# Kernel optimization log

Measured on AMD Instinct MI355X. Metric: run time of the kernel, lower is better.

The kernel has to match this reference:

```python
import jax, jax.numpy as jnp
import numpy as np

B, N, D = 32, 4096, 256
H, DH, S = 8, 64, 16
DI = H * DH          # dim_inner = 512
HID = 1024           # max(dim, hidden_dim)
ITERS = 3
EPS = 1e-8
SCALE = D ** (-0.5)  # NOTE: original uses dim, not dim_head


def _ln(x, g, b):
    m = jnp.mean(x, axis=-1, keepdims=True)
    v = jnp.mean((x - m) ** 2, axis=-1, keepdims=True)
    return (x - m) * jax.lax.rsqrt(v + 1e-5) * g + b


def _lin(x, W, b):  # torch layout: W [out, in]
    return x @ W.T + b


def setup_inputs() -> dict:
    key = jax.random.key(0)
    ks = jax.random.split(key, 32)

    def p(i, shape, s=0.02):
        return jax.random.normal(ks[i], shape, dtype=jnp.float32) * s

    return {
        "x": jax.random.normal(ks[0], (B, N, D), dtype=jnp.float32),
        "slots_noise": jax.random.normal(ks[1], (B, S, D), dtype=jnp.float32),
        "slots_mu": p(2, (1, 1, D), 1.0),
        "slots_logsigma": p(3, (1, 1, D)),
        "ln_in_g": jnp.ones((D,), jnp.float32), "ln_in_b": jnp.zeros((D,), jnp.float32),
        "ln_s_g": jnp.ones((D,), jnp.float32), "ln_s_b": jnp.zeros((D,), jnp.float32),
        "ln_ff_g": jnp.ones((D,), jnp.float32), "ln_ff_b": jnp.zeros((D,), jnp.float32),
        "Wq": p(4, (DI, D)), "bq": jnp.zeros((DI,), jnp.float32),
        "Wk": p(5, (DI, D)), "bk": jnp.zeros((DI,), jnp.float32),
        "Wv": p(6, (DI, D)), "bv": jnp.zeros((DI,), jnp.float32),
        "Wc": p(7, (D, DI)), "bc": jnp.zeros((D,), jnp.float32),
        "gru_wih": p(8, (3 * D, D)), "gru_whh": p(9, (3 * D, D)),
        "gru_bih": jnp.zeros((3 * D,), jnp.float32), "gru_bhh": jnp.zeros((3 * D,), jnp.float32),
        "W1": p(10, (HID, D)), "b1": jnp.zeros((HID,), jnp.float32),
        "W2": p(11, (D, HID)), "b2": jnp.zeros((D,), jnp.float32),
    }


def reference(x, slots_noise, slots_mu, slots_logsigma,
              ln_in_g, ln_in_b, ln_s_g, ln_s_b, ln_ff_g, ln_ff_b,
              Wq, bq, Wk, bk, Wv, bv, Wc, bc,
              gru_wih, gru_whh, gru_bih, gru_bhh,
              W1, b1, W2, b2):
    slots = slots_mu + jnp.exp(slots_logsigma) * slots_noise  # [B,S,D]
    xn = _ln(x, ln_in_g, ln_in_b)
    k = _lin(xn, Wk, bk).reshape(B, N, H, DH)  # [B,N,H,DH]
    v = _lin(xn, Wv, bv).reshape(B, N, H, DH)

    for _ in range(ITERS):
        slots_prev = slots
        sn = _ln(slots, ln_s_g, ln_s_b)
        q = _lin(sn, Wq, bq).reshape(B, S, H, DH)             # [B,S,H,DH]
        logits = jnp.einsum('bihd,bjhd->bhij', q, k) * SCALE  # [B,H,S,N]
        attn = jax.nn.softmax(logits, axis=-1) + EPS
        attn = attn / jnp.sum(attn, axis=-1, keepdims=True)
        upd = jnp.einsum('bhij,bjhd->bihd', attn, v).reshape(B, S, DI)
        upd = _lin(upd, Wc, bc)                               # [B,S,D]
        # GRUCell (torch gate order r, z, n)
        gi = _lin(upd.reshape(-1, D), gru_wih, gru_bih)
        gh = _lin(slots_prev.reshape(-1, D), gru_whh, gru_bhh)
        ir, iz, inn = jnp.split(gi, 3, axis=-1)
        hr, hz, hn = jnp.split(gh, 3, axis=-1)
        r = jax.nn.sigmoid(ir + hr)
        z = jax.nn.sigmoid(iz + hz)
        n = jnp.tanh(inn + r * hn)
        slots = ((1.0 - z) * n + z * slots_prev.reshape(-1, D)).reshape(B, S, D)
        slots = slots + _lin(jax.nn.relu(_lin(_ln(slots, ln_ff_g, ln_ff_b), W1, b1)), W2, b2)
    return slots
```

## Files before the change

kernel.cpp:

```cpp
#include <hip/hip_runtime.h>
#include <stdint.h>

#define B_   32
#define N_   4096
#define D_   256
#define H_   8
#define S_   16
#define DI_  512
#define HID_ 1024
#define CH_  8
#define NCHUNK_ 512
#define SCALE_ 0.0625f

typedef short  short8 __attribute__((ext_vector_type(8)));
typedef float  f32x4  __attribute__((ext_vector_type(4)));

__device__ __forceinline__ unsigned short f2bf(float x){
  union { float f; unsigned u; } v; v.f = x;
  unsigned r = v.u + 0x7FFFu + ((v.u >> 16) & 1u);
  return (unsigned short)(r >> 16);
}

__device__ __forceinline__ void gld16(const void* g, void* l){
  __builtin_amdgcn_global_load_lds(
      (const __attribute__((address_space(1))) unsigned int*)g,
      (__attribute__((address_space(3))) unsigned int*)l, 16, 0, 0);
}

#define FMA4(acc, a, Wm) do { (acc)[0] += (a)*(Wm).x; (acc)[1] += (a)*(Wm).y; (acc)[2] += (a)*(Wm).z; (acc)[3] += (a)*(Wm).w; } while(0)

__global__ void k_badws(float* out){ out[blockIdx.x*256 + threadIdx.x] = 1e9f; }

__global__ __launch_bounds__(256) void k_init_slots(
    const float* __restrict__ noise, const float* __restrict__ mu,
    const float* __restrict__ lsig, float* __restrict__ slots)
{
  int i = blockIdx.x*256 + threadIdx.x;
  int d = i & 255;
  slots[i] = mu[d] + expf(lsig[d]) * noise[i];
}

__global__ __launch_bounds__(256) void k_transpose(
    const float* __restrict__ src, float* __restrict__ dst, int R, int C)
{
  __shared__ float t[32][33];
  int c0 = blockIdx.x*32, r0 = blockIdx.y*32;
  int tx = threadIdx.x, ty = threadIdx.y;
  for (int j = 0; j < 32; j += 8){
    int r = r0 + ty + j, c = c0 + tx;
    if (r < R && c < C) t[ty+j][tx] = src[(size_t)r*C + c];
  }
  __syncthreads();
  for (int j = 0; j < 32; j += 8){
    int c = c0 + ty + j, r = r0 + tx;
    if (c < C && r < R) dst[(size_t)c*R + r] = t[tx][ty+j];
  }
}

__global__ __launch_bounds__(256) void k_ln_x(
    const float* __restrict__ x, const float* __restrict__ g, const float* __restrict__ bb,
    unsigned short* __restrict__ xn, unsigned short* __restrict__ xnT)
{
  __shared__ __align__(16) char tile[32768];
  const int blk = blockIdx.x;
  const int b  = blk >> 6;
  const int n0 = (blk & 63) * 64;
  const int t = threadIdx.x;
  const int lane = t & 63;
  const int w = t >> 6;
  float4 gv = *(const float4*)&g[lane*4];
  float4 bv = *(const float4*)&bb[lane*4];
#pragma unroll 1
  for (int it = 0; it < 16; ++it){
    const int nl = w*16 + it;
    const size_t row = (size_t)b*N_ + n0 + nl;
    float4 xv = *(const float4*)&x[row*256 + lane*4];
    float s = xv.x + xv.y + xv.z + xv.w;
    float q = xv.x*xv.x + xv.y*xv.y + xv.z*xv.z + xv.w*xv.w;
#pragma unroll
    for (int m = 1; m < 64; m <<= 1){ s += __shfl_xor(s, m); q += __shfl_xor(q, m); }
    float mean = s * 0.00390625f;
    float var  = q * 0.00390625f - mean*mean;
    float rs = rsqrtf(var + 1e-5f);
    unsigned short u0 = f2bf((xv.x-mean)*rs*gv.x + bv.x);
    unsigned short u1 = f2bf((xv.y-mean)*rs*gv.y + bv.y);
    unsigned short u2 = f2bf((xv.z-mean)*rs*gv.z + bv.z);
    unsigned short u3 = f2bf((xv.w-mean)*rs*gv.w + bv.w);
    uint2 pk; pk.x = (unsigned)u0 | ((unsigned)u1 << 16); pk.y = (unsigned)u2 | ((unsigned)u3 << 16);
    *(uint2*)&xn[row*256 + lane*4] = pk;
    *(uint2*)(tile + nl*512 + ((lane*8) ^ ((nl & 7) << 4))) = pk;
  }
  __syncthreads();
#pragma unroll 1
  for (int j = 0; j < 32; ++j){
    int flat = j*256 + t;
    int d  = flat >> 5;
    int np = (flat & 31) * 2;
    unsigned short lo = *(const unsigned short*)(tile + np*512     + ((2*d) ^ ((np     & 7) << 4)));
    unsigned short hi = *(const unsigned short*)(tile + (np+1)*512 + ((2*d) ^ (((np+1) & 7) << 4)));
    *(unsigned*)&xnT[((size_t)b*D_ + d)*N_ + n0 + np] = (unsigned)lo | ((unsigned)hi << 16);
  }
}

__global__ __launch_bounds__(256) void k_preA(
    const float* __restrict__ slots, const float* __restrict__ lsg, const float* __restrict__ lsb,
    const float* __restrict__ WqT, const float* __restrict__ bq, float* __restrict__ ql)
{
  __shared__ __align__(16) float a[4][256];
  const int lane = threadIdx.x & 63, w = threadIdx.x >> 6;
  const int row = blockIdx.x*4 + w;
  const int o   = blockIdx.y*64 + lane;
  float4 v = *(const float4*)&slots[(size_t)row*D_ + lane*4];
  float s = v.x + v.y + v.z + v.w;
  float q = v.x*v.x + v.y*v.y + v.z*v.z + v.w*v.w;
#pragma unroll
  for (int m = 1; m < 64; m <<= 1){ s += __shfl_xor(s, m); q += __shfl_xor(q, m); }
  float mean = s * 0.00390625f;
  float var  = q * 0.00390625f - mean*mean;
  float rs = rsqrtf(var + 1e-5f);
  float4 gv = *(const float4*)&lsg[lane*4];
  float4 bv = *(const float4*)&lsb[lane*4];
  a[w][lane*4+0] = (v.x-mean)*rs*gv.x + bv.x;
  a[w][lane*4+1] = (v.y-mean)*rs*gv.y + bv.y;
  a[w][lane*4+2] = (v.z-mean)*rs*gv.z + bv.z;
  a[w][lane*4+3] = (v.w-mean)*rs*gv.w + bv.w;
  const float* Wp = WqT + o;
  float acc = 0.f;
#pragma unroll 4
  for (int k4 = 0; k4 < 64; ++k4){
    float4 av = *(const float4*)&a[w][k4*4];
    acc += av.x * Wp[(size_t)(k4*4+0)*512];
    acc += av.y * Wp[(size_t)(k4*4+1)*512];
    acc += av.z * Wp[(size_t)(k4*4+2)*512];
    acc += av.w * Wp[(size_t)(k4*4+3)*512];
  }
  ql[(size_t)row*DI_ + o] = acc + bq[o];
}

__global__ __launch_bounds__(256) void k_preB(
    const float* __restrict__ ql, const float* __restrict__ Wk, const float* __restrict__ bk,
    unsigned short* __restrict__ qp, float* __restrict__ qb)
{
  __shared__ __align__(16) float qs[16][64];
  const int id = blockIdx.x;
  const int b  = id >> 3;
  const int h  = id & 7;
  const int cb = blockIdx.y;
  const int c0 = cb*64;
  const int t = threadIdx.x;
  const int lane = t & 63, w = t >> 6;
  {
    int flat = t*4;
    int s = flat >> 6, k = flat & 63;
    *(float4*)&qs[s][k] = *(const float4*)&ql[((size_t)(b*S_ + s))*DI_ + h*64 + k];
  }
  __syncthreads();
  if (cb == 0){
    float bkv = bk[h*64 + lane];
#pragma unroll
    for (int r = 0; r < 4; ++r){
      int s = w*4 + r;
      float v = qs[s][lane] * bkv;
#pragma unroll
      for (int m = 1; m < 64; m <<= 1) v += __shfl_xor(v, m);
      if (lane == 0) qb[((size_t)b*H_ + h)*S_ + s] = v * SCALE_;
    }
  }
  float acc[4] = {};
  const float* Wp = Wk + (size_t)(h*64)*256 + c0 + lane;
#pragma unroll 4
  for (int k = 0; k < 64; ++k){
    float wv = Wp[(size_t)k*256];
    acc[0] += qs[w*4+0][k] * wv;
    acc[1] += qs[w*4+1][k] * wv;
    acc[2] += qs[w*4+2][k] * wv;
    acc[3] += qs[w*4+3][k] * wv;
  }
#pragma unroll
  for (int r = 0; r < 4; ++r){
    int s = w*4 + r;
    qp[(((size_t)b*H_ + h)*S_ + s)*D_ + c0 + lane] = f2bf(SCALE_ * acc[r]);
  }
}

__global__ __launch_bounds__(512, 2) void k_flash(
    const unsigned short* __restrict__ xn, const unsigned short* __restrict__ xnT,
    const unsigned short* __restrict__ qp, const float* __restrict__ qb,
    float* __restrict__ mPart, float* __restrict__ lPart, float* __restrict__ axPart)
{
  __shared__ __align__(16) char lds[147456];
  const int ch = blockIdx.x;
  const int b  = blockIdx.y;
  const int t  = threadIdx.x;
  const int lane = t & 63;
  const int w  = t >> 6;
  const int g  = lane >> 4;
  const int c  = lane & 15;
  const int n0 = ch * NCHUNK_;

  short8 aq[8];
#pragma unroll
  for (int ks = 0; ks < 8; ++ks)
    aq[ks] = *(const short8*)&qp[(((size_t)b*H_ + w)*S_ + c)*D_ + ks*32 + g*8];
  float qbr[4];
#pragma unroll
  for (int r = 0; r < 4; ++r)
    qbr[r] = qb[((size_t)b*H_ + w)*S_ + g*4 + r];

  f32x4 accX[16];
#pragma unroll
  for (int i = 0; i < 16; ++i){ f32x4 z = {0.f,0.f,0.f,0.f}; accX[i] = z; }
  float mrun[4] = {-1e30f,-1e30f,-1e30f,-1e30f};
  float lrun[4] = {0.f,0.f,0.f,0.f};

  auto ISSUE = [&](int tl, int buf){
    char* lb = lds + buf*65536;
#pragma unroll
    for (int j = 0; j < 4; ++j){
      int rl = w*8 + j*2 + (lane >> 5);
      int cs = (lane & 31) ^ (rl & 7);
      gld16(&xn[((size_t)b*N_ + n0 + tl*64 + rl)*D_ + cs*8],
            lb + (w*8 + j*2)*512);
    }
#pragma unroll
    for (int j = 0; j < 4; ++j){
      int dl = w*32 + j*8 + (lane >> 3);
      int cs = (lane & 7) ^ (dl & 7);
      gld16(&xnT[((size_t)b*D_ + dl)*N_ + n0 + tl*64 + cs*8],
            lb + 32768 + (w*32 + j*8)*128);
    }
  };

  ISSUE(0, 0);
  __syncthreads();
  int cur = 0;
#pragma unroll 1
  for (int tl = 0; tl < 8; ++tl){
    if (tl < 7) ISSUE(tl + 1, cur ^ 1);
    const char* xb  = lds + cur*65536;
    const char* xbT = lds + cur*65536 + 32768;
    char* pbuf = lds + 131072 + w*2048;
    f32x4 lg[4];
#pragma unroll
    for (int nf = 0; nf < 4; ++nf){ f32x4 z = {0.f,0.f,0.f,0.f}; lg[nf] = z; }
#pragma unroll
    for (int ks = 0; ks < 8; ++ks){
#pragma unroll
      for (int nf = 0; nf < 4; ++nf){
        int n = nf*16 + c;
        short8 bf = *(const short8*)(xb + n*512 + (((ks*32 + g*8)*2) ^ ((n & 7) << 4)));
        lg[nf] = __builtin_amdgcn_mfma_f32_16x16x32_bf16(aq[ks], bf, lg[nf], 0, 0, 0);
      }
    }
    float tmax[4];
#pragma unroll
    for (int r = 0; r < 4; ++r){
      lg[0][r] += qbr[r]; lg[1][r] += qbr[r]; lg[2][r] += qbr[r]; lg[3][r] += qbr[r];
      tmax[r] = fmaxf(fmaxf(lg[0][r], lg[1][r]), fmaxf(lg[2][r], lg[3][r]));
      tmax[r] = fmaxf(tmax[r], __shfl_xor(tmax[r], 1));
      tmax[r] = fmaxf(tmax[r], __shfl_xor(tmax[r], 2));
      tmax[r] = fmaxf(tmax[r], __shfl_xor(tmax[r], 4));
      tmax[r] = fmaxf(tmax[r], __shfl_xor(tmax[r], 8));
    }
    float fac[4], psum[4];
#pragma unroll
    for (int r = 0; r < 4; ++r){
      float mnew = fmaxf(mrun[r], tmax[r]);
      fac[r] = __expf(mrun[r] - mnew);
      mrun[r] = mnew;
      lrun[r] *= fac[r];
      psum[r] = 0.f;
    }
#pragma unroll
    for (int i = 0; i < 16; ++i){
      accX[i][0] *= fac[0]; accX[i][1] *= fac[1]; accX[i][2] *= fac[2]; accX[i][3] *= fac[3];
    }
#pragma unroll
    for (int nf = 0; nf < 4; ++nf){
#pragma unroll
      for (int r = 0; r < 4; ++r){
        float p = __expf(lg[nf][r] - mrun[r]);
        psum[r] += p;
        int row = g*4 + r;
        *(unsigned short*)(pbuf + row*128 + (((nf*16 + c)*2) ^ ((row & 7) << 4))) = f2bf(p);
      }
    }
#pragma unroll
    for (int r = 0; r < 4; ++r){
      psum[r] += __shfl_xor(psum[r], 1);
      psum[r] += __shfl_xor(psum[r], 2);
      psum[r] += __shfl_xor(psum[r], 4);
      psum[r] += __shfl_xor(psum[r], 8);
      lrun[r] += psum[r];
    }
#pragma unroll
    for (int ks = 0; ks < 2; ++ks){
      short8 pa = *(const short8*)(pbuf + c*128 + (((ks*32 + g*8)*2) ^ ((c & 7) << 4)));
#pragma unroll
      for (int df = 0; df < 16; ++df){
        int d = df*16 + c;
        short8 bt = *(const short8*)(xbT + d*128 + (((ks*32 + g*8)*2) ^ ((d & 7) << 4)));
        accX[df] = __builtin_amdgcn_mfma_f32_16x16x32_bf16(pa, bt, accX[df], 0, 0, 0);
      }
    }
    __syncthreads();
    cur ^= 1;
  }
  size_t base = (((size_t)b*CH_ + ch)*H_ + w)*S_;
  if (c == 0){
#pragma unroll
    for (int r = 0; r < 4; ++r){
      mPart[base + g*4 + r] = mrun[r];
      lPart[base + g*4 + r] = lrun[r];
    }
  }
  size_t base3 = base * D_;
#pragma unroll
  for (int df = 0; df < 16; ++df){
#pragma unroll
    for (int r = 0; r < 4; ++r){
      axPart[base3 + df*256 + r*64 + lane] = accX[df][r];
    }
  }
}

__global__ __launch_bounds__(256) void k_combine(
    const float* __restrict__ mPart, const float* __restrict__ lPart, const float* __restrict__ axPart,
    const float* __restrict__ WvT, const float* __restrict__ bv, float* __restrict__ upd)
{
  __shared__ __align__(16) float av[4][256];
  const int id = blockIdx.x;
  const int b  = id >> 5;
  const int h  = (id >> 2) & 7;
  const int sq = id & 3;
  const int t = threadIdx.x;
  const int sl = t >> 6;
  const int lane = t & 63;
  const int s = sq*4 + sl;
  const int sg = s >> 2, sr = s & 3;
  const size_t pb = (((size_t)b*CH_)*H_ + h)*S_ + s;
  float mg = -1e30f;
  float mv[8], lv[8];
#pragma unroll
  for (int k = 0; k < 8; ++k){
    mv[k] = mPart[pb + (size_t)k*128];
    lv[k] = lPart[pb + (size_t)k*128];
    mg = fmaxf(mg, mv[k]);
  }
  const size_t off_s = (size_t)sr*64 + sg*16 + (lane>>2)*256 + (lane&3)*4;
  float L = 0.f, ax0 = 0.f, ax1 = 0.f, ax2 = 0.f, ax3 = 0.f;
#pragma unroll
  for (int k = 0; k < 8; ++k){
    float wgt = __expf(mv[k] - mg);
    L += lv[k]*wgt;
    size_t base3 = ((((size_t)b*CH_ + k)*H_ + h)*S_) * D_;
    float4 a4 = *(const float4*)&axPart[base3 + off_s];
    ax0 += a4.x*wgt; ax1 += a4.y*wgt; ax2 += a4.z*wgt; ax3 += a4.w*wgt;
  }
  float inv = 1.f / L;
  av[sl][lane*4+0] = ax0*inv; av[sl][lane*4+1] = ax1*inv;
  av[sl][lane*4+2] = ax2*inv; av[sl][lane*4+3] = ax3*inv;
  __syncthreads();
  float acc = bv[h*64 + lane];
  for (int d = 0; d < 256; d += 2){
    float2 a2 = *(const float2*)&av[sl][d];
    acc += a2.x * WvT[(size_t)d*512     + h*64 + lane];
    acc += a2.y * WvT[(size_t)(d+1)*512 + h*64 + lane];
  }
  upd[((size_t)b*S_ + s)*DI_ + h*64 + lane] = acc;
}

__global__ __launch_bounds__(256) void k_sA(
    const float* __restrict__ upd, const float* __restrict__ WcT,
    const float* __restrict__ bc, float* __restrict__ updc)
{
  __shared__ __align__(16) float act[4][512];
  const int lane = threadIdx.x & 63, w = threadIdx.x >> 6;
  const int row = blockIdx.x*4 + w;
  const int col = blockIdx.y*64 + lane;
  *(float4*)&act[w][lane*8]     = *(const float4*)&upd[(size_t)row*DI_ + lane*8];
  *(float4*)&act[w][lane*8 + 4] = *(const float4*)&upd[(size_t)row*DI_ + lane*8 + 4];
  const float* Wp = WcT + col;
  float acc = 0.f;
#pragma unroll 4
  for (int k4 = 0; k4 < 128; ++k4){
    float4 a = *(const float4*)&act[w][k4*4];
    acc += a.x * Wp[(size_t)(k4*4+0)*256];
    acc += a.y * Wp[(size_t)(k4*4+1)*256];
    acc += a.z * Wp[(size_t)(k4*4+2)*256];
    acc += a.w * Wp[(size_t)(k4*4+3)*256];
  }
  updc[(size_t)row*D_ + col] = acc + bc[col];
}

__global__ __launch_bounds__(256) void k_sB(
    const float* __restrict__ updc, const float* __restrict__ slots,
    const float* __restrict__ wihT, const float* __restrict__ whhT,
    const float* __restrict__ bih, const float* __restrict__ bhh,
    float* __restrict__ snl)
{
  __shared__ __align__(16) float au[4][256];
  __shared__ __align__(16) float as[4][256];
  const int lane = threadIdx.x & 63, w = threadIdx.x >> 6;
  const int row = blockIdx.x*4 + w;
  const int d   = blockIdx.y*64 + lane;
  *(float4*)&au[w][lane*4] = *(const float4*)&updc[(size_t)row*D_ + lane*4];
  *(float4*)&as[w][lane*4] = *(const float4*)&slots[(size_t)row*D_ + lane*4];
  const float* Wi = wihT + d;
  const float* Wh = whhT + d;
  float air=0.f, aiz=0.f, ain=0.f, ahr=0.f, ahz=0.f, ahn=0.f;
#pragma unroll 2
  for (int k4 = 0; k4 < 64; ++k4){
    float4 u = *(const float4*)&au[w][k4*4];
    float4 s = *(const float4*)&as[w][k4*4];
#pragma unroll
    for (int j = 0; j < 4; ++j){
      int k = k4*4 + j;
      float uv = (j==0)?u.x:(j==1)?u.y:(j==2)?u.z:u.w;
      float sv = (j==0)?s.x:(j==1)?s.y:(j==2)?s.z:s.w;
      air += uv * Wi[(size_t)k*768];
      aiz += uv * Wi[(size_t)k*768 + 256];
      ain += uv * Wi[(size_t)k*768 + 512];
      ahr += sv * Wh[(size_t)k*768];
      ahz += sv * Wh[(size_t)k*768 + 256];
      ahn += sv * Wh[(size_t)k*768 + 512];
    }
  }
  float ir = air + bih[d]     + ahr + bhh[d];
  float iz = aiz + bih[256+d] + ahz + bhh[256+d];
  float rg = 1.f/(1.f + __expf(-ir));
  float zg = 1.f/(1.f + __expf(-iz));
  float ng = tanhf(ain + bih[512+d] + rg*(ahn + bhh[512+d]));
  snl[(size_t)row*D_ + d] = (1.f - zg)*ng + zg*as[w][d];
}

__global__ __launch_bounds__(256) void k_sC(
    const float* __restrict__ snl, const float* __restrict__ lfg, const float* __restrict__ lfb,
    const float* __restrict__ W1T, const float* __restrict__ b1, float* __restrict__ h1)
{
  __shared__ __align__(16) float a[4][256];
  const int lane = threadIdx.x & 63, w = threadIdx.x >> 6;
  const int row = blockIdx.x*4 + w;
  const int o   = blockIdx.y*64 + lane;
  float4 v = *(const float4*)&snl[(size_t)row*D_ + lane*4];
  float s = v.x + v.y + v.z + v.w;
  float q = v.x*v.x + v.y*v.y + v.z*v.z + v.w*v.w;
#pragma unroll
  for (int m = 1; m < 64; m <<= 1){ s += __shfl_xor(s, m); q += __shfl_xor(q, m); }
  float mean = s * 0.00390625f;
  float var  = q * 0.00390625f - mean*mean;
  float rs = rsqrtf(var + 1e-5f);
  float4 gv = *(const float4*)&lfg[lane*4];
  float4 bv = *(const float4*)&lfb[lane*4];
  a[w][lane*4+0] = (v.x-mean)*rs*gv.x + bv.x;
  a[w][lane*4+1] = (v.y-mean)*rs*gv.y + bv.y;
  a[w][lane*4+2] = (v.z-mean)*rs*gv.z + bv.z;
  a[w][lane*4+3] = (v.w-mean)*rs*gv.w + bv.w;
  const float* Wp = W1T + o;
  float acc = 0.f;
#pragma unroll 4
  for (int k4 = 0; k4 < 64; ++k4){
    float4 av = *(const float4*)&a[w][k4*4];
    acc += av.x * Wp[(size_t)(k4*4+0)*1024];
    acc += av.y * Wp[(size_t)(k4*4+1)*1024];
    acc += av.z * Wp[(size_t)(k4*4+2)*1024];
    acc += av.w * Wp[(size_t)(k4*4+3)*1024];
  }
  h1[(size_t)row*HID_ + o] = fmaxf(acc + b1[o], 0.f);
}

__global__ __launch_bounds__(256) void k_sD(
    const float* __restrict__ h1, const float* __restrict__ snl,
    const float* __restrict__ W2T, const float* __restrict__ b2, float* __restrict__ dst)
{
  __shared__ __align__(16) float a[4][1024];
  const int lane = threadIdx.x & 63, w = threadIdx.x >> 6;
  const int row = blockIdx.x*4 + w;
  const int o   = blockIdx.y*64 + lane;
#pragma unroll
  for (int j = 0; j < 4; ++j)
    *(float4*)&a[w][lane*16 + j*4] = *(const float4*)&h1[(size_t)row*HID_ + lane*16 + j*4];
  const float* Wp = W2T + o;
  float acc = 0.f;
#pragma unroll 4
  for (int k4 = 0; k4 < 256; ++k4){
    float4 av = *(const float4*)&a[w][k4*4];
    acc += av.x * Wp[(size_t)(k4*4+0)*256];
    acc += av.y * Wp[(size_t)(k4*4+1)*256];
    acc += av.z * Wp[(size_t)(k4*4+2)*256];
    acc += av.w * Wp[(size_t)(k4*4+3)*256];
  }
  dst[(size_t)row*D_ + o] = snl[(size_t)row*D_ + o] + acc + b2[o];
}

extern "C" void kernel_launch(void* const* d_in, const int* in_sizes, int n_in,
                              void* d_out, int out_size, void* d_ws, size_t ws_size,
                              hipStream_t stream)
{
  const float* x       = (const float*)d_in[0];
  const float* noise   = (const float*)d_in[1];
  const float* mu      = (const float*)d_in[2];
  const float* lsig    = (const float*)d_in[3];
  const float* ln_in_g = (const float*)d_in[4];
  const float* ln_in_b = (const float*)d_in[5];
  const float* ln_s_g  = (const float*)d_in[6];
  const float* ln_s_b  = (const float*)d_in[7];
  const float* ln_ff_g = (const float*)d_in[8];
  const float* ln_ff_b = (const float*)d_in[9];
  const float* Wq  = (const float*)d_in[10]; const float* bq  = (const float*)d_in[11];
  const float* Wk  = (const float*)d_in[12]; const float* bk  = (const float*)d_in[13];
  const float* Wv  = (const float*)d_in[14]; const float* bv  = (const float*)d_in[15];
  const float* Wc  = (const float*)d_in[16]; const float* bc  = (const float*)d_in[17];
  const float* wih = (const float*)d_in[18]; const float* whh = (const float*)d_in[19];
  const float* bih = (const float*)d_in[20]; const float* bhh = (const float*)d_in[21];
  const float* W1  = (const float*)d_in[22]; const float* b1  = (const float*)d_in[23];
  const float* W2  = (const float*)d_in[24]; const float* b2  = (const float*)d_in[25];

  char* ws = (char*)d_ws;
  unsigned short* xn  = (unsigned short*)(ws + 0);
  unsigned short* xnT = (unsigned short*)(ws + 67108864);
  float* slots = (float*)(ws + 134217728);
  unsigned short* qp = (unsigned short*)(ws + 134742016);
  float* qb   = (float*)(ws + 136839168);
  float* mP   = (float*)(ws + 136855552);
  float* lP   = (float*)(ws + 136986624);
  float* axP  = (float*)(ws + 137117696);
  float* upd  = (float*)(ws + 170672128);
  float* WqT  = (float*)(ws + 171720704);
  float* WvT  = (float*)(ws + 172244992);
  float* WcT  = (float*)(ws + 172769280);
  float* wihT = (float*)(ws + 173293568);
  float* whhT = (float*)(ws + 174080000);
  float* W1T  = (float*)(ws + 174866432);
  float* W2T  = (float*)(ws + 175915008);
  float* updc = (float*)(ws + 137117696);
  float* snl  = (float*)(ws + 137641984);
  float* h1   = (float*)(ws + 138166272);
  float* ql   = (float*)(ws + 141000704);

  if (ws_size < (size_t)176963584ull){
    k_badws<<<512, 256, 0, stream>>>((float*)d_out);
    return;
  }

  k_init_slots<<<512, 256, 0, stream>>>(noise, mu, lsig, slots);
  k_ln_x<<<2048, 256, 0, stream>>>(x, ln_in_g, ln_in_b, xn, xnT);
  dim3 tb(32, 8);
  k_transpose<<<dim3(8, 16), tb, 0, stream>>>(Wq,  WqT,  512,  256);
  k_transpose<<<dim3(8, 16), tb, 0, stream>>>(Wv,  WvT,  512,  256);
  k_transpose<<<dim3(16, 8), tb, 0, stream>>>(Wc,  WcT,  256,  512);
  k_transpose<<<dim3(8, 24), tb, 0, stream>>>(wih, wihT, 768,  256);
  k_transpose<<<dim3(8, 24), tb, 0, stream>>>(whh, whhT, 768,  256);
  k_transpose<<<dim3(8, 32), tb, 0, stream>>>(W1,  W1T,  1024, 256);
  k_transpose<<<dim3(32, 8), tb, 0, stream>>>(W2,  W2T,  256,  1024);

  for (int it = 0; it < 3; ++it){
    k_preA<<<dim3(128, 8), 256, 0, stream>>>(slots, ln_s_g, ln_s_b, WqT, bq, ql);
    k_preB<<<dim3(256, 4), 256, 0, stream>>>(ql, Wk, bk, qp, qb);
    k_flash<<<dim3(CH_, B_), 512, 0, stream>>>(xn, xnT, qp, qb, mP, lP, axP);
    k_combine<<<1024, 256, 0, stream>>>(mP, lP, axP, WvT, bv, upd);
    k_sA<<<dim3(128, 4),  256, 0, stream>>>(upd, WcT, bc, updc);
    k_sB<<<dim3(128, 4),  256, 0, stream>>>(updc, slots, wihT, whhT, bih, bhh, snl);
    k_sC<<<dim3(128, 16), 256, 0, stream>>>(snl, ln_ff_g, ln_ff_b, W1T, b1, h1);
    k_sD<<<dim3(128, 4),  256, 0, stream>>>(h1, snl, W2T, b2, (it == 2) ? (float*)d_out : slots);
  }
}
```

Measured before the change: 577.6 us.

## Single-buffer flash LDS for two blocks per CU; merge weight transposes

Shrinks the flash kernel's shared memory from 144KB to 80KB by dropping the double buffer. The next tile's load is now issued after the compute and a barrier, so two 512-thread blocks can share a CU. The cost is that loads no longer overlap compute within a block, and the design relies on the second resident block to hide that latency. Separately, the seven weight-transpose launches are merged into one kernel that picks its matrix from the block index, cutting launch overhead.

```diff
diff --git a/kernel.cpp b/kernel.cpp
--- a/kernel.cpp
+++ b/kernel.cpp
@@ -27,8 +27,6 @@
       (__attribute__((address_space(3))) unsigned int*)l, 16, 0, 0);
 }
 
-#define FMA4(acc, a, Wm) do { (acc)[0] += (a)*(Wm).x; (acc)[1] += (a)*(Wm).y; (acc)[2] += (a)*(Wm).z; (acc)[3] += (a)*(Wm).w; } while(0)
-
 __global__ void k_badws(float* out){ out[blockIdx.x*256 + threadIdx.x] = 1e9f; }
 
 __global__ __launch_bounds__(256) void k_init_slots(
@@ -40,11 +38,25 @@
   slots[i] = mu[d] + expf(lsig[d]) * noise[i];
 }
 
-__global__ __launch_bounds__(256) void k_transpose(
-    const float* __restrict__ src, float* __restrict__ dst, int R, int C)
+__global__ __launch_bounds__(256) void k_tr_all(
+    const float* __restrict__ Wq,  const float* __restrict__ Wv,  const float* __restrict__ Wc,
+    const float* __restrict__ wih, const float* __restrict__ whh,
+    const float* __restrict__ W1,  const float* __restrict__ W2,
+    float* __restrict__ WqT, float* __restrict__ WvT, float* __restrict__ WcT,
+    float* __restrict__ wihT, float* __restrict__ whhT,
+    float* __restrict__ W1T, float* __restrict__ W2T)
 {
   __shared__ float t[32][33];
-  int c0 = blockIdx.x*32, r0 = blockIdx.y*32;
+  const int id = blockIdx.x;
+  const float* src; float* dst; int R, C, bx, by;
+  if      (id < 128) { src=Wq;  dst=WqT;  R=512;  C=256;  int s=id;      bx=s&7;  by=s>>3; }
+  else if (id < 256) { src=Wv;  dst=WvT;  R=512;  C=256;  int s=id-128;  bx=s&7;  by=s>>3; }
+  else if (id < 384) { src=Wc;  dst=WcT;  R=256;  C=512;  int s=id-256;  bx=s&15; by=s>>4; }
+  else if (id < 576) { src=wih; dst=wihT; R=768;  C=256;  int s=id-384;  bx=s&7;  by=s>>3; }
+  else if (id < 768) { src=whh; dst=whhT; R=768;  C=256;  int s=id-576;  bx=s&7;  by=s>>3; }
+  else if (id < 1024){ src=W1;  dst=W1T;  R=1024; C=256;  int s=id-768;  bx=s&7;  by=s>>3; }
+  else               { src=W2;  dst=W2T;  R=256;  C=1024; int s=id-1024; bx=s&31; by=s>>5; }
+  int c0 = bx*32, r0 = by*32;
   int tx = threadIdx.x, ty = threadIdx.y;
   for (int j = 0; j < 32; j += 8){
     int r = r0 + ty + j, c = c0 + tx;
@@ -188,7 +200,7 @@
     const unsigned short* __restrict__ qp, const float* __restrict__ qb,
     float* __restrict__ mPart, float* __restrict__ lPart, float* __restrict__ axPart)
 {
-  __shared__ __align__(16) char lds[147456];
+  __shared__ __align__(16) char lds[81920];
   const int ch = blockIdx.x;
   const int b  = blockIdx.y;
   const int t  = threadIdx.x;
@@ -213,33 +225,30 @@
   float mrun[4] = {-1e30f,-1e30f,-1e30f,-1e30f};
   float lrun[4] = {0.f,0.f,0.f,0.f};
 
-  auto ISSUE = [&](int tl, int buf){
-    char* lb = lds + buf*65536;
+  auto ISSUE = [&](int tl){
 #pragma unroll
     for (int j = 0; j < 4; ++j){
       int rl = w*8 + j*2 + (lane >> 5);
       int cs = (lane & 31) ^ (rl & 7);
       gld16(&xn[((size_t)b*N_ + n0 + tl*64 + rl)*D_ + cs*8],
-            lb + (w*8 + j*2)*512);
+            lds + (w*8 + j*2)*512);
     }
 #pragma unroll
     for (int j = 0; j < 4; ++j){
       int dl = w*32 + j*8 + (lane >> 3);
       int cs = (lane & 7) ^ (dl & 7);
       gld16(&xnT[((size_t)b*D_ + dl)*N_ + n0 + tl*64 + cs*8],
-            lb + 32768 + (w*32 + j*8)*128);
+            lds + 32768 + (w*32 + j*8)*128);
     }
   };
 
-  ISSUE(0, 0);
-  __syncthreads();
-  int cur = 0;
+  ISSUE(0);
 #pragma unroll 1
   for (int tl = 0; tl < 8; ++tl){
-    if (tl < 7) ISSUE(tl + 1, cur ^ 1);
-    const char* xb  = lds + cur*65536;
-    const char* xbT = lds + cur*65536 + 32768;
-    char* pbuf = lds + 131072 + w*2048;
+    __syncthreads();
+    const char* xb  = lds;
+    const char* xbT = lds + 32768;
+    char* pbuf = lds + 65536 + w*2048;
     f32x4 lg[4];
 #pragma unroll
     for (int nf = 0; nf < 4; ++nf){ f32x4 z = {0.f,0.f,0.f,0.f}; lg[nf] = z; }
@@ -304,7 +313,7 @@
       }
     }
     __syncthreads();
-    cur ^= 1;
+    if (tl < 7) ISSUE(tl + 1);
   }
   size_t base = (((size_t)b*CH_ + ch)*H_ + w)*S_;
   if (c == 0){
@@ -545,14 +554,8 @@
 
   k_init_slots<<<512, 256, 0, stream>>>(noise, mu, lsig, slots);
   k_ln_x<<<2048, 256, 0, stream>>>(x, ln_in_g, ln_in_b, xn, xnT);
-  dim3 tb(32, 8);
-  k_transpose<<<dim3(8, 16), tb, 0, stream>>>(Wq,  WqT,  512,  256);
-  k_transpose<<<dim3(8, 16), tb, 0, stream>>>(Wv,  WvT,  512,  256);
-  k_transpose<<<dim3(16, 8), tb, 0, stream>>>(Wc,  WcT,  256,  512);
-  k_transpose<<<dim3(8, 24), tb, 0, stream>>>(wih, wihT, 768,  256);
-  k_transpose<<<dim3(8, 24), tb, 0, stream>>>(whh, whhT, 768,  256);
-  k_transpose<<<dim3(8, 32), tb, 0, stream>>>(W1,  W1T,  1024, 256);
-  k_transpose<<<dim3(32, 8), tb, 0, stream>>>(W2,  W2T,  256,  1024);
+  k_tr_all<<<1280, dim3(32, 8), 0, stream>>>(Wq, Wv, Wc, wih, whh, W1, W2,
+                                             WqT, WvT, WcT, wihT, whhT, W1T, W2T);
 
   for (int it = 0; it < 3; ++it){
     k_preA<<<dim3(128, 8), 256, 0, stream>>>(slots, ln_s_g, ln_s_b, WqT, bq, ql);
```

Result: faster. 561.9 us, median of 2 (-2.7%).
